# Kernel optimization log

Hardware: AMD Instinct MI355X
Metric: run time of the kernel (lower is better)

Reference implementation:

```python
import jax, jax.numpy as jnp
import numpy as np

MARGIN = 0.3
PD_EPS = 1e-6  # torch.nn.functional.pairwise_distance default eps (added to the diff)


def setup_inputs() -> dict:
    key = jax.random.key(0)
    k1, k2 = jax.random.split(key)
    n, d = 8192, 128
    inputs = jax.random.normal(k1, (n, d), dtype=jnp.float32)
    positive = jax.random.normal(k2, (n, d), dtype=jnp.float32)
    return {"inputs": inputs, "positive": positive}


def reference(inputs, positive):
    # Pairwise squared Euclidean distances: ||xi||^2 + ||xj||^2 - 2 xi.xj  -> [n, n]
    sq = jnp.sum(inputs * inputs, axis=1, keepdims=True)  # [n, 1]
    dist = sq + sq.T - 2.0 * (inputs @ inputs.T)
    dist = jnp.sqrt(jnp.clip(dist, 1e-12, None))

    # Original: dist[i].argsort()[4] -> 5th-nearest (index 0 is self at ~0 distance).
    # Equivalent, avoiding full per-row sort: top-5 smallest distances.
    _, idx = jax.lax.top_k(-dist, 5)  # idx: [n, 5], ascending by distance
    negative = inputs[idx[:, 4]]  # hard negatives, [n, d]

    # TripletMarginLoss(margin=0.3, p=2): pairwise_distance adds eps to the diff.
    d_ap = jnp.linalg.norm(inputs - positive + PD_EPS, axis=1)
    d_an = jnp.linalg.norm(inputs - negative + PD_EPS, axis=1)
    return jnp.mean(jnp.maximum(d_ap - d_an + MARGIN, 0.0))
```

## Files before the change

### kernel.cpp

```cpp
#include <hip/hip_runtime.h>

#define NN 8192
#define DD 128
#define CH 16
#define CPC (NN / CH)
#define TILES (CPC / 64)

typedef __bf16 bf16x8 __attribute__((ext_vector_type(8)));
typedef float f32x4 __attribute__((ext_vector_type(4)));

#define PACK_INIT __uint_as_float(0x7F7FFFFFu)

static __device__ __forceinline__ float packsi(float s, unsigned idx) {
  return __uint_as_float((__float_as_uint(s) & 0xFFFFE000u) | idx);
}

static __device__ __forceinline__ void net5(float& s0, float& s1, float& s2,
                                            float& s3, float& s4, float v) {
  float t1 = fmaxf(s0, v);  s0 = fminf(s0, v);
  float t2 = fmaxf(s1, t1); s1 = fminf(s1, t1);
  float t3 = fmaxf(s2, t2); s2 = fminf(s2, t2);
  float t4 = fmaxf(s3, t3); s3 = fminf(s3, t3);
  s4 = fminf(s4, t4);
}

static __device__ __forceinline__ unsigned short f2bf(float f) {
  unsigned u = __float_as_uint(f);
  u += 0x7FFFu + ((u >> 16) & 1u);
  return (unsigned short)(u >> 16);
}

__global__ __launch_bounds__(256) void prep_kernel(const float* __restrict__ x,
                                                   unsigned short* __restrict__ xb,
                                                   float* __restrict__ sq,
                                                   float* __restrict__ out) {
  const int wave = threadIdx.x >> 6, lane = threadIdx.x & 63;
  const int row = blockIdx.x * 4 + wave;
  const float2 v = ((const float2*)(x + (size_t)row * DD))[lane];
  float ss = v.x * v.x + v.y * v.y;
#pragma unroll
  for (int off = 32; off; off >>= 1) ss += __shfl_down(ss, off);
  if (lane == 0) sq[row] = ss;
  unsigned packed = (unsigned)f2bf(v.x) | ((unsigned)f2bf(v.y) << 16);
  ((unsigned*)(xb + (size_t)row * DD))[lane] = packed;
  if (blockIdx.x == 0 && threadIdx.x == 0) out[0] = 0.0f;
}

__global__ __launch_bounds__(256, 4) void dist_topk_kernel(
    const unsigned short* __restrict__ xb, const float* __restrict__ sq,
    float* __restrict__ pscore) {
  const int t = threadIdx.x;
  const int wave = t >> 6, lane = t & 63;
  const int lrow = lane & 15, lquad = lane >> 4;
  const int rowBase = blockIdx.x * 128;
  const int chunk = blockIdx.y;
  const int j0 = chunk * CPC;

  __shared__ unsigned short colsB[2][64 * DD];
  __shared__ float sqs[2][64];

  const int myrow0 = rowBase + wave * 32 + lrow;
  const int myrow1 = myrow0 + 16;
  const unsigned short* ap0 = xb + (size_t)myrow0 * DD + lquad * 8;
  const unsigned short* ap1 = xb + (size_t)myrow1 * DD + lquad * 8;
  bf16x8 a00 = *(const bf16x8*)(ap0);
  bf16x8 a01 = *(const bf16x8*)(ap0 + 32);
  bf16x8 a02 = *(const bf16x8*)(ap0 + 64);
  bf16x8 a03 = *(const bf16x8*)(ap0 + 96);
  bf16x8 a10 = *(const bf16x8*)(ap1);
  bf16x8 a11 = *(const bf16x8*)(ap1 + 32);
  bf16x8 a12 = *(const bf16x8*)(ap1 + 64);
  bf16x8 a13 = *(const bf16x8*)(ap1 + 96);

  float p00 = PACK_INIT, p01 = PACK_INIT, p02 = PACK_INIT, p03 = PACK_INIT,
        p04 = PACK_INIT;
  float p10 = PACK_INIT, p11 = PACK_INIT, p12 = PACK_INIT, p13 = PACK_INIT,
        p14 = PACK_INIT;

  const int sr = t >> 4, sch = t & 15;
  const int dst0 = (sr << 4) | (sch ^ (sr & 15));

  const float4* srcv = (const float4*)(xb + (size_t)j0 * DD);
  float4 g0 = srcv[t], g1 = srcv[t + 256], g2 = srcv[t + 512], g3 = srcv[t + 768];
  float sqv = 0.0f;
  if (t < 64) sqv = sq[j0 + t];

  for (int it = 0; it < TILES; ++it) {
    const int jt = j0 + it * 64;
    const int cur = it & 1;
    {
      float4* dstv = (float4*)colsB[cur];
      dstv[dst0] = g0;
      dstv[dst0 + 256] = g1;
      dstv[dst0 + 512] = g2;
      dstv[dst0 + 768] = g3;
      if (t < 64) sqs[cur][t] = sqv;
    }
    if (it + 1 < TILES) {
      const float4* nsrc = (const float4*)(xb + (size_t)(jt + 64) * DD);
      g0 = nsrc[t]; g1 = nsrc[t + 256]; g2 = nsrc[t + 512]; g3 = nsrc[t + 768];
      if (t < 64) sqv = sq[jt + 64 + t];
    }
    __syncthreads();

#pragma unroll
    for (int ct = 0; ct < 4; ++ct) {
      const unsigned short* bb = &colsB[cur][(ct * 16 + lrow) * DD];
      bf16x8 b0 = *(const bf16x8*)(bb + (((0 + lquad) ^ lrow) << 3));
      bf16x8 b1 = *(const bf16x8*)(bb + (((4 + lquad) ^ lrow) << 3));
      bf16x8 b2 = *(const bf16x8*)(bb + (((8 + lquad) ^ lrow) << 3));
      bf16x8 b3 = *(const bf16x8*)(bb + (((12 + lquad) ^ lrow) << 3));
      f32x4 acc0 = {0.f, 0.f, 0.f, 0.f};
      f32x4 acc1 = {0.f, 0.f, 0.f, 0.f};
      acc0 = __builtin_amdgcn_mfma_f32_16x16x32_bf16(b0, a00, acc0, 0, 0, 0);
      acc1 = __builtin_amdgcn_mfma_f32_16x16x32_bf16(b0, a10, acc1, 0, 0, 0);
      acc0 = __builtin_amdgcn_mfma_f32_16x16x32_bf16(b1, a01, acc0, 0, 0, 0);
      acc1 = __builtin_amdgcn_mfma_f32_16x16x32_bf16(b1, a11, acc1, 0, 0, 0);
      acc0 = __builtin_amdgcn_mfma_f32_16x16x32_bf16(b2, a02, acc0, 0, 0, 0);
      acc1 = __builtin_amdgcn_mfma_f32_16x16x32_bf16(b2, a12, acc1, 0, 0, 0);
      acc0 = __builtin_amdgcn_mfma_f32_16x16x32_bf16(b3, a03, acc0, 0, 0, 0);
      acc1 = __builtin_amdgcn_mfma_f32_16x16x32_bf16(b3, a13, acc1, 0, 0, 0);
      const f32x4 sq4 = *(const f32x4*)&sqs[cur][ct * 16 + lquad * 4];
      const unsigned colb = (unsigned)(jt + ct * 16 + lquad * 4);
#pragma unroll
      for (int r = 0; r < 4; ++r) {
        net5(p00, p01, p02, p03, p04, packsi(fmaf(-2.0f, acc0[r], sq4[r]), colb + r));
        net5(p10, p11, p12, p13, p14, packsi(fmaf(-2.0f, acc1[r], sq4[r]), colb + r));
      }
    }
  }

#pragma unroll
  for (int m = 16; m < 64; m <<= 1) {
    float o0 = __shfl_xor(p00, m), o1 = __shfl_xor(p01, m), o2 = __shfl_xor(p02, m),
          o3 = __shfl_xor(p03, m), o4 = __shfl_xor(p04, m);
    net5(p00, p01, p02, p03, p04, o0);
    net5(p00, p01, p02, p03, p04, o1);
    net5(p00, p01, p02, p03, p04, o2);
    net5(p00, p01, p02, p03, p04, o3);
    net5(p00, p01, p02, p03, p04, o4);
    o0 = __shfl_xor(p10, m); o1 = __shfl_xor(p11, m); o2 = __shfl_xor(p12, m);
    o3 = __shfl_xor(p13, m); o4 = __shfl_xor(p14, m);
    net5(p10, p11, p12, p13, p14, o0);
    net5(p10, p11, p12, p13, p14, o1);
    net5(p10, p11, p12, p13, p14, o2);
    net5(p10, p11, p12, p13, p14, o3);
    net5(p10, p11, p12, p13, p14, o4);
  }
  if (lquad == 0) {
    const size_t b0i = ((size_t)chunk * NN + myrow0) * 5;
    pscore[b0i + 0] = p00; pscore[b0i + 1] = p01; pscore[b0i + 2] = p02;
    pscore[b0i + 3] = p03; pscore[b0i + 4] = p04;
    const size_t b1i = ((size_t)chunk * NN + myrow1) * 5;
    pscore[b1i + 0] = p10; pscore[b1i + 1] = p11; pscore[b1i + 2] = p12;
    pscore[b1i + 3] = p13; pscore[b1i + 4] = p14;
  }
}

__global__ __launch_bounds__(256) void final_kernel(const float* __restrict__ x,
                                                    const float* __restrict__ pos,
                                                    const float* __restrict__ pscore,
                                                    float* __restrict__ out) {
  const int wave = threadIdx.x >> 6, lane = threadIdx.x & 63;
  const int row = blockIdx.x * 4 + wave;

  float q0 = PACK_INIT, q1 = PACK_INIT, q2 = PACK_INIT, q3 = PACK_INIT,
        q4 = PACK_INIT;
  if (lane < CH) {
    const float* b = pscore + ((size_t)lane * NN + row) * 5;
    q0 = b[0]; q1 = b[1]; q2 = b[2]; q3 = b[3]; q4 = b[4];
  }
#pragma unroll
  for (int m = 1; m < CH; m <<= 1) {
    float o0 = __shfl_xor(q0, m), o1 = __shfl_xor(q1, m), o2 = __shfl_xor(q2, m),
          o3 = __shfl_xor(q3, m), o4 = __shfl_xor(q4, m);
    net5(q0, q1, q2, q3, q4, o0);
    net5(q0, q1, q2, q3, q4, o1);
    net5(q0, q1, q2, q3, q4, o2);
    net5(q0, q1, q2, q3, q4, o3);
    net5(q0, q1, q2, q3, q4, o4);
  }
  const int nidx = (int)(__float_as_uint(__shfl(q4, 0)) & 0x1FFFu);

  const float2 xv  = ((const float2*)(x   + (size_t)row  * DD))[lane];
  const float2 pv  = ((const float2*)(pos + (size_t)row  * DD))[lane];
  const float2 nvv = ((const float2*)(x   + (size_t)nidx * DD))[lane];
  float a0 = xv.x - pv.x + 1e-6f, a1 = xv.y - pv.y + 1e-6f;
  float b0 = xv.x - nvv.x + 1e-6f, b1 = xv.y - nvv.y + 1e-6f;
  float dap = a0 * a0 + a1 * a1;
  float dan = b0 * b0 + b1 * b1;
#pragma unroll
  for (int off = 32; off; off >>= 1) {
    dap += __shfl_down(dap, off);
    dan += __shfl_down(dan, off);
  }
  __shared__ float hs[4];
  if (lane == 0) hs[wave] = fmaxf(sqrtf(dap) - sqrtf(dan) + 0.3f, 0.0f);
  __syncthreads();
  if (threadIdx.x == 0) {
    float s = hs[0] + hs[1] + hs[2] + hs[3];
    atomicAdd(out, s * (1.0f / 8192.0f));
  }
}

extern "C" void kernel_launch(void* const* d_in, const int* in_sizes, int n_in,
                              void* d_out, int out_size, void* d_ws, size_t ws_size,
                              hipStream_t stream) {
  const float* x   = (const float*)d_in[0];
  const float* pos = (const float*)d_in[1];
  float* out = (float*)d_out;

  char* w = (char*)d_ws;
  unsigned short* xb = (unsigned short*)w;
  float* sq = (float*)(w + (size_t)NN * DD * 2);
  float* pscore = (float*)(w + (size_t)NN * DD * 2 + (size_t)NN * 4);

  prep_kernel<<<NN / 4, 256, 0, stream>>>(x, xb, sq, out);
  dist_topk_kernel<<<dim3(NN / 128, CH), 256, 0, stream>>>(xb, sq, pscore);
  final_kernel<<<NN / 4, 256, 0, stream>>>(x, pos, pscore, out);
}
```

Measured before the change: 123.6 us.

## Load B tiles directly from global memory instead of staging through LDS

After: 156.2 us. 26.3% more time.

```diff
diff --git a/kernel.cpp b/kernel.cpp
--- a/kernel.cpp
+++ b/kernel.cpp
@@ -56,9 +56,6 @@
   const int chunk = blockIdx.y;
   const int j0 = chunk * CPC;
 
-  __shared__ unsigned short colsB[2][64 * DD];
-  __shared__ float sqs[2][64];
-
   const int myrow0 = rowBase + wave * 32 + lrow;
   const int myrow1 = myrow0 + 16;
   const unsigned short* ap0 = xb + (size_t)myrow0 * DD + lquad * 8;
@@ -77,39 +74,19 @@
   float p10 = PACK_INIT, p11 = PACK_INIT, p12 = PACK_INIT, p13 = PACK_INIT,
         p14 = PACK_INIT;
 
-  const int sr = t >> 4, sch = t & 15;
-  const int dst0 = (sr << 4) | (sch ^ (sr & 15));
-
-  const float4* srcv = (const float4*)(xb + (size_t)j0 * DD);
-  float4 g0 = srcv[t], g1 = srcv[t + 256], g2 = srcv[t + 512], g3 = srcv[t + 768];
-  float sqv = 0.0f;
-  if (t < 64) sqv = sq[j0 + t];
+  const unsigned short* bbase = xb + (size_t)(j0 + lrow) * DD + lquad * 8;
+  const float* sqbase = sq + j0 + lquad * 4;
 
   for (int it = 0; it < TILES; ++it) {
-    const int jt = j0 + it * 64;
-    const int cur = it & 1;
-    {
-      float4* dstv = (float4*)colsB[cur];
-      dstv[dst0] = g0;
-      dstv[dst0 + 256] = g1;
-      dstv[dst0 + 512] = g2;
-      dstv[dst0 + 768] = g3;
-      if (t < 64) sqs[cur][t] = sqv;
-    }
-    if (it + 1 < TILES) {
-      const float4* nsrc = (const float4*)(xb + (size_t)(jt + 64) * DD);
-      g0 = nsrc[t]; g1 = nsrc[t + 256]; g2 = nsrc[t + 512]; g3 = nsrc[t + 768];
-      if (t < 64) sqv = sq[jt + 64 + t];
-    }
-    __syncthreads();
-
+    const int jt = it * 64;
 #pragma unroll
     for (int ct = 0; ct < 4; ++ct) {
-      const unsigned short* bb = &colsB[cur][(ct * 16 + lrow) * DD];
-      bf16x8 b0 = *(const bf16x8*)(bb + (((0 + lquad) ^ lrow) << 3));
-      bf16x8 b1 = *(const bf16x8*)(bb + (((4 + lquad) ^ lrow) << 3));
-      bf16x8 b2 = *(const bf16x8*)(bb + (((8 + lquad) ^ lrow) << 3));
-      bf16x8 b3 = *(const bf16x8*)(bb + (((12 + lquad) ^ lrow) << 3));
+      const unsigned short* bp = bbase + (size_t)(jt + ct * 16) * DD;
+      bf16x8 b0 = *(const bf16x8*)(bp);
+      bf16x8 b1 = *(const bf16x8*)(bp + 32);
+      bf16x8 b2 = *(const bf16x8*)(bp + 64);
+      bf16x8 b3 = *(const bf16x8*)(bp + 96);
+      const f32x4 sq4 = *(const f32x4*)(sqbase + jt + ct * 16);
       f32x4 acc0 = {0.f, 0.f, 0.f, 0.f};
       f32x4 acc1 = {0.f, 0.f, 0.f, 0.f};
       acc0 = __builtin_amdgcn_mfma_f32_16x16x32_bf16(b0, a00, acc0, 0, 0, 0);
@@ -120,8 +97,7 @@
       acc1 = __builtin_amdgcn_mfma_f32_16x16x32_bf16(b2, a12, acc1, 0, 0, 0);
       acc0 = __builtin_amdgcn_mfma_f32_16x16x32_bf16(b3, a03, acc0, 0, 0, 0);
       acc1 = __builtin_amdgcn_mfma_f32_16x16x32_bf16(b3, a13, acc1, 0, 0, 0);
-      const f32x4 sq4 = *(const f32x4*)&sqs[cur][ct * 16 + lquad * 4];
-      const unsigned colb = (unsigned)(jt + ct * 16 + lquad * 4);
+      const unsigned colb = (unsigned)(j0 + jt + ct * 16 + lquad * 4);
 #pragma unroll
       for (int r = 0; r < 4; ++r) {
         net5(p00, p01, p02, p03, p04, packsi(fmaf(-2.0f, acc0[r], sq4[r]), colb + r));
```
